# Performance work log

Measured on AMD Instinct MI355X. Metric: run time of the kernel, lower is better.

Reference implementation:

```python
import jax, jax.numpy as jnp
from jax import lax
import numpy as np

D_MODEL = 96; D_STATE = 16; SSM_RATIO = 2.0; D_CONV = 3; K = 4
D_INNER = int(SSM_RATIO * D_MODEL)      # 192
DT_RANK = -(-D_MODEL // 16)             # ceil(96/16) = 6
B_SZ = 4; H = 32; W = 32

# ---- zig-zag (snake) index helpers (static numpy) ----
def _snake_h(Hh, Ww):
    idx = np.tile(np.arange(Ww), (Hh, 1)); idx[1::2] = idx[1::2, ::-1]; return idx  # (H,W)

def _snake_v(Hh, Ww):
    idx = np.tile(np.arange(Hh)[:, None], (1, Ww)); idx[:, 1::2] = idx[::-1, 1::2]; return idx  # (H,W)

def _h_scan(x, d):
    Hh, Ww = x.shape[-2:]
    if d == 'left':
        x = jnp.flip(x, (-1, -2))
    return x[:, :, np.arange(Hh)[:, None], _snake_h(Hh, Ww)]

def _v_scan(x, d):
    Bb, Cc, Hh, Ww = x.shape
    if d == 'up':
        x = jnp.flip(x, (-1, -2))
    t = x[:, :, _snake_v(Hh, Ww), np.arange(Ww)[None, :]]  # gather along H per column
    return jnp.swapaxes(t, -1, -2).reshape(Bb, Cc, Hh, Ww)

def _h_merge(x, d):
    Hh, Ww = x.shape[-2:]
    t = x[:, :, np.arange(Hh)[:, None], _snake_h(Hh, Ww)]
    if d == 'left':
        t = jnp.flip(t, (-1, -2))
    return t

def _v_merge(x, d):
    Hh, Ww = x.shape[-2:]
    t2 = jnp.swapaxes(x, -1, -2)  # (B,C,W,H); requires H==W like the torch source
    t = t2[:, :, _snake_v(Hh, Ww), np.arange(Ww)[None, :]]
    if d == 'up':
        t = jnp.flip(t, (-1, -2))
    return t

def cross_scan(x):
    return jnp.stack([_v_scan(x, 'down'), _v_scan(x, 'up'), _h_scan(x, 'right'), _h_scan(x, 'left')], axis=1)

def cross_merge(ys):
    return (_v_merge(ys[:, 0], 'down') + _v_merge(ys[:, 1], 'up')
            + _h_merge(ys[:, 2], 'right') + _h_merge(ys[:, 3], 'left'))

def selective_scan(u, delta, A, Bs, Cs, Dp, delta_bias):
    # u,delta:(B,K,D,L)  A:(K,D,N)  Bs,Cs:(B,K,N,L)  Dp,delta_bias:(K,D)
    delta = jax.nn.softplus(delta + delta_bias[None, :, :, None])
    dA = jnp.exp(jnp.einsum('bkdl,kdn->lbkdn', delta, A))
    dBu = jnp.einsum('bkdl,bkdl,bknl->lbkdn', delta, u, Bs)
    Ct = jnp.moveaxis(Cs, -1, 0)  # (L,B,K,N)
    def step(h, inp):
        dA_t, dBu_t, c_t = inp
        h = dA_t * h + dBu_t
        return h, jnp.einsum('bkdn,bkn->bkd', h, c_t)
    h0 = jnp.zeros(dA.shape[1:], u.dtype)
    _, ys = lax.scan(step, h0, (dA, dBu, Ct))
    return jnp.moveaxis(ys, 0, -1) + Dp[None, :, :, None] * u  # (B,K,D,L)

def setup_inputs() -> dict:
    key = jax.random.key(0)
    ks = jax.random.split(key, 8)
    x = jax.random.normal(ks[0], (B_SZ, D_MODEL, H, W), jnp.float32)
    in_proj_w = jax.random.normal(ks[1], (2 * D_INNER, D_MODEL), jnp.float32) * (D_MODEL ** -0.5)
    conv_w = jax.random.normal(ks[2], (D_INNER, 1, D_CONV, D_CONV), jnp.float32) * 0.2  # depthwise
    conv_b = jnp.zeros((D_INNER,), jnp.float32)
    x_proj_w = jax.random.normal(ks[3], (K, DT_RANK + 2 * D_STATE, D_INNER), jnp.float32) * (D_INNER ** -0.5)
    s = DT_RANK ** -0.5
    dt_w = jax.random.uniform(ks[4], (K, D_INNER, DT_RANK), jnp.float32, -s, s)
    dt = jax.random.uniform(ks[5], (K, D_INNER), jnp.float32, 0.001, 0.1)
    dt_b = jnp.log(jnp.expm1(dt))  # inverse softplus, as in dt_init
    A_logs = jnp.tile(jnp.log(jnp.arange(1, D_STATE + 1, dtype=jnp.float32)), (K * D_INNER, 1))
    Ds = jnp.ones((K * D_INNER,), jnp.float32)
    gn_gamma = jnp.ones((D_INNER,), jnp.float32)
    gn_beta = jnp.zeros((D_INNER,), jnp.float32)
    out_proj_w = jax.random.normal(ks[6], (D_MODEL, D_INNER), jnp.float32) * (D_INNER ** -0.5)
    return {'x': x, 'in_proj_w': in_proj_w, 'conv_w': conv_w, 'conv_b': conv_b,
            'x_proj_w': x_proj_w, 'dt_w': dt_w, 'dt_b': dt_b, 'A_logs': A_logs, 'Ds': Ds,
            'gn_gamma': gn_gamma, 'gn_beta': gn_beta, 'out_proj_w': out_proj_w}

def reference(x, in_proj_w, conv_w, conv_b, x_proj_w, dt_w, dt_b, A_logs, Ds, gn_gamma, gn_beta, out_proj_w):
    Bb, _, Hh, Ww = x.shape; L = Hh * Ww
    xz = jnp.einsum('bchw,oc->bohw', x, in_proj_w)          # in_proj (1x1 conv, no bias)
    xx, z = jnp.split(xz, 2, axis=1)
    z = jax.nn.silu(z)
    xx = lax.conv_general_dilated(xx, conv_w, (1, 1), 'SAME', feature_group_count=D_INNER,
                                  dimension_numbers=('NCHW', 'OIHW', 'NCHW')) + conv_b[None, :, None, None]
    xx = jax.nn.silu(xx)
    xs = cross_scan(xx).reshape(Bb, K, D_INNER, L)          # 4-direction zig-zag scan
    x_dbl = jnp.einsum('bkdl,kcd->bkcl', xs, x_proj_w)
    dts = jnp.einsum('bkrl,kdr->bkdl', x_dbl[:, :, :DT_RANK], dt_w)
    Bs = x_dbl[:, :, DT_RANK:DT_RANK + D_STATE]
    Cs = x_dbl[:, :, DT_RANK + D_STATE:]
    A = -jnp.exp(A_logs).reshape(K, D_INNER, D_STATE)
    y = selective_scan(xs, dts, A, Bs, Cs, Ds.reshape(K, D_INNER), dt_b)
    y = cross_merge(y.reshape(Bb, K, D_INNER, Hh, Ww))       # (B,D,H,W)
    # out_norm: GroupNorm(1, d_inner) == layernorm over (C,H,W) per sample
    mu = jnp.mean(y, axis=(1, 2, 3), keepdims=True)
    var = jnp.var(y, axis=(1, 2, 3), keepdims=True)
    y = (y - mu) * lax.rsqrt(var + 1e-6)
    y = y * gn_gamma[None, :, None, None] + gn_beta[None, :, None, None]
    y = y * z
    return jnp.einsum('bchw,oc->bohw', y, out_proj_w)
```

## Files before the change

### kernel.cpp

```cpp
#include <hip/hip_runtime.h>
#include <math.h>

#define Bsz 4
#define DM 96
#define DI 192
#define NS 16
#define RK 6
#define KK 4
#define HH 32
#define WW 32
#define LL 1024
#define NC 32
#define CS 32

__device__ __forceinline__ float silu_f(float x) { return x / (1.f + __expf(-x)); }

__device__ __forceinline__ int hw_of_l(int k, int l) {
    int a = l >> 5, r = l & 31;
    int m = (a & 1) ? 31 - r : r;
    int h, w;
    if (k < 2) { w = a; h = m; }
    else       { h = a; w = m; }
    if (k & 1) { h = 31 - h; w = 31 - w; }
    return h * 32 + w;
}

__global__ void in_proj_k(const float* __restrict__ x, const float* __restrict__ w,
                          float* __restrict__ xx, float* __restrict__ zs,
                          float* __restrict__ stats) {
    int bi = blockIdx.x;
    int t = threadIdx.x;
    if (bi == 0 && t < 2 * Bsz) stats[t] = 0.f;
    int lb = bi & 3;
    int og = (bi >> 2) % 96;
    int b = bi / 384;
    int l = lb * 256 + t;
    const float* xb = x + (size_t)b * DM * LL + l;
    float acc[4];
#pragma unroll
    for (int g = 0; g < 4; g++) acc[g] = 0.f;
    for (int c = 0; c < DM; c++) {
        float xv = xb[(size_t)c * LL];
#pragma unroll
        for (int g = 0; g < 4; g++)
            acc[g] = fmaf(xv, w[(size_t)(og * 4 + g) * DM + c], acc[g]);
    }
#pragma unroll
    for (int g = 0; g < 4; g++) {
        int o = og * 4 + g;
        if (o < DI) xx[((size_t)b * DI + o) * LL + l] = acc[g];
        else        zs[((size_t)b * DI + (o - DI)) * LL + l] = silu_f(acc[g]);
    }
}

__global__ void convT_k(const float* __restrict__ xx, const float* __restrict__ cw,
                        const float* __restrict__ cb, float* __restrict__ xxT) {
    __shared__ float tile[32][33];
    int bi = blockIdx.x;
    int h0 = bi % 32;
    int dt = (bi / 32) % 6;
    int b = bi / 192;
    int d0 = dt * 32;
    int t = threadIdx.x;
    int wi = t & 31, dg = t >> 5;

#pragma unroll
    for (int pass = 0; pass < 4; pass++) {
        int di = pass * 8 + dg;
        int d = d0 + di;
        const float* xp = xx + ((size_t)b * DI + d) * LL;
        const float* wp = cw + d * 9;
        float acc = cb[d];
#pragma unroll
        for (int kh = 0; kh < 3; kh++) {
            int hh = h0 + kh - 1;
            if (hh < 0 || hh >= HH) continue;
#pragma unroll
            for (int kw = 0; kw < 3; kw++) {
                int ww2 = wi + kw - 1;
                if (ww2 < 0 || ww2 >= WW) continue;
                acc = fmaf(xp[hh * WW + ww2], wp[kh * 3 + kw], acc);
            }
        }
        tile[wi][di] = silu_f(acc);
    }
    __syncthreads();

    int di = t & 31, w8 = t >> 5;
#pragma unroll
    for (int rep = 0; rep < 4; rep++) {
        int w2 = rep * 8 + w8;
        xxT[((size_t)b * LL + h0 * 32 + w2) * DI + d0 + di] = tile[w2][di];
    }
}

__global__ void __launch_bounds__(512)
xdbl_k(const float* __restrict__ xxT, const float* __restrict__ xpw,
       float* __restrict__ xdbl) {
    __shared__ float tile[64 * 193];
    int blk = blockIdx.x;
    int bk = blk >> 4, lt = blk & 15;
    int k = bk & 3, b = bk >> 2;
    int t = threadIdx.x;

    const float* xb = xxT + (size_t)b * LL * DI;
#pragma unroll
    for (int i = 0; i < 6; i++) {
        int j4 = t + i * 512;
        int lr = j4 / 48;
        int d4 = j4 % 48;
        int hw = hw_of_l(k, lt * 64 + lr);
        float4 v = ((const float4*)(xb + (size_t)hw * DI))[d4];
        float* dst = &tile[lr * 193 + d4 * 4];
        dst[0] = v.x; dst[1] = v.y; dst[2] = v.z; dst[3] = v.w;
    }
    __syncthreads();

    int ll = t & 63;
    int cg = t >> 6;
    int c0 = cg * 5;
    int wlim = (c0 + 5 <= 38) ? 5 : (38 - c0);
    const float* wk = xpw + (size_t)k * 38 * DI;

    float acc[5];
#pragma unroll
    for (int j = 0; j < 5; j++) acc[j] = 0.f;
    const float* xrow = &tile[ll * 193];
#pragma unroll 4
    for (int d = 0; d < DI; d++) {
        float xv = xrow[d];
#pragma unroll
        for (int j = 0; j < 5; j++) {
            int cc = c0 + j; cc = (cc > 37) ? 37 : cc;
            acc[j] = fmaf(xv, wk[(size_t)cc * DI + d], acc[j]);
        }
    }
    float* orow = xdbl + ((size_t)bk * LL + lt * 64 + ll) * 38;
#pragma unroll
    for (int j = 0; j < 5; j++)
        if (j < wlim) orow[c0 + j] = acc[j];
}

#define XDP 40

__global__ void scan_p1(const float* __restrict__ xxT, const float* __restrict__ xdbl,
                        const float* __restrict__ dtw_g, const float* __restrict__ dtb_g,
                        const float* __restrict__ Alog,
                        float* __restrict__ Pst, float* __restrict__ Hloc) {
    __shared__ float u_tile[CS * 192];
    __shared__ float xd_tile[CS * XDP];
    int blk = blockIdx.x;
    int bk = blk / NC, c = blk % NC;
    int k = bk & 3, b = bk >> 2;
    int t = threadIdx.x;

    const float* xb = xxT + (size_t)b * LL * DI;
#pragma unroll
    for (int i = 0; i < 8; i++) {
        int j4 = t + i * 192;
        int s = j4 / 48, d4 = j4 % 48;
        int hw = hw_of_l(k, c * CS + s);
        float4 v = ((const float4*)(xb + (size_t)hw * DI))[d4];
        ((float4*)(&u_tile[s * 192]))[d4] = v;
    }
    const float* xdsrc = xdbl + ((size_t)bk * LL + c * CS) * 38;
    for (int i = t; i < CS * 38; i += 192) {
        int s = i / 38, j = i - s * 38;
        int pj = (j < 6) ? 32 + j : j - 6;
        xd_tile[s * XDP + pj] = xdsrc[i];
    }
    __syncthreads();

    int d = t;
    int kd = k * DI + d;
    float A0 = -__expf(Alog[(size_t)kd * NS]);
    bool pw = true;
#pragma unroll
    for (int n = 1; n < NS; n++) {
        float An = -__expf(Alog[(size_t)kd * NS + n]);
        pw = pw && (fabsf(An - (float)(n + 1) * A0) <= 1e-4f * (float)(n + 1));
    }
    float dtw[RK];
#pragma unroll
    for (int r = 0; r < RK; r++) dtw[r] = dtw_g[(size_t)kd * RK + r];
    float dtb = dtb_g[kd];

    float h[NS], P[NS];
#pragma unroll
    for (int n = 0; n < NS; n++) h[n] = 0.f;

    if (pw) {
        float R = 1.f;
        for (int s = 0; s < CS; s++) {
            const float4* xr = (const float4*)(&xd_tile[s * XDP]);
            float4 b0 = xr[0], b1 = xr[1], b2 = xr[2], b3 = xr[3];
            float4 q0 = xr[8], q1 = xr[9];
            float bb[16];
            bb[0]=b0.x; bb[1]=b0.y; bb[2]=b0.z; bb[3]=b0.w;
            bb[4]=b1.x; bb[5]=b1.y; bb[6]=b1.z; bb[7]=b1.w;
            bb[8]=b2.x; bb[9]=b2.y; bb[10]=b2.z; bb[11]=b2.w;
            bb[12]=b3.x; bb[13]=b3.y; bb[14]=b3.z; bb[15]=b3.w;
            float dt = dtb;
            dt = fmaf(q0.x, dtw[0], dt); dt = fmaf(q0.y, dtw[1], dt);
            dt = fmaf(q0.z, dtw[2], dt); dt = fmaf(q0.w, dtw[3], dt);
            dt = fmaf(q1.x, dtw[4], dt); dt = fmaf(q1.y, dtw[5], dt);
            dt = (dt > 20.f) ? dt : __logf(1.f + __expf(dt));
            float du = dt * u_tile[s * 192 + d];
            float r1 = __expf(dt * A0);
            float r2 = r1 * r1, r4 = r2 * r2, r8 = r4 * r4;
            float aa[16];
            aa[0] = r1; aa[1] = r2; aa[2] = r1 * r2; aa[3] = r4;
#pragma unroll
            for (int n = 0; n < 4; n++) aa[n + 4] = aa[n] * r4;
#pragma unroll
            for (int n = 0; n < 8; n++) aa[n + 8] = aa[n] * r8;
#pragma unroll
            for (int n = 0; n < NS; n++) h[n] = fmaf(aa[n], h[n], du * bb[n]);
            R *= r1;
        }
        float R2 = R * R, R4 = R2 * R2, R8 = R4 * R4;
        P[0] = R; P[1] = R2; P[2] = R * R2; P[3] = R4;
#pragma unroll
        for (int n = 0; n < 4; n++) P[n + 4] = P[n] * R4;
        P[7] = R8;
#pragma unroll
        for (int n = 0; n < 8; n++) P[n + 8] = P[n] * R8;
    } else {
        float A[NS];
#pragma unroll
        for (int n = 0; n < NS; n++) A[n] = -__expf(Alog[(size_t)kd * NS + n]);
#pragma unroll
        for (int n = 0; n < NS; n++) P[n] = 1.f;
        for (int s = 0; s < CS; s++) {
            const float4* xr = (const float4*)(&xd_tile[s * XDP]);
            float4 b0 = xr[0], b1 = xr[1], b2 = xr[2], b3 = xr[3];
            float4 q0 = xr[8], q1 = xr[9];
            float bb[16];
            bb[0]=b0.x; bb[1]=b0.y; bb[2]=b0.z; bb[3]=b0.w;
            bb[4]=b1.x; bb[5]=b1.y; bb[6]=b1.z; bb[7]=b1.w;
            bb[8]=b2.x; bb[9]=b2.y; bb[10]=b2.z; bb[11]=b2.w;
            bb[12]=b3.x; bb[13]=b3.y; bb[14]=b3.z; bb[15]=b3.w;
            float dt = dtb;
            dt = fmaf(q0.x, dtw[0], dt); dt = fmaf(q0.y, dtw[1], dt);
            dt = fmaf(q0.z, dtw[2], dt); dt = fmaf(q0.w, dtw[3], dt);
            dt = fmaf(q1.x, dtw[4], dt); dt = fmaf(q1.y, dtw[5], dt);
            dt = (dt > 20.f) ? dt : __logf(1.f + __expf(dt));
            float du = dt * u_tile[s * 192 + d];
#pragma unroll
            for (int n = 0; n < NS; n++) {
                float a = __expf(dt * A[n]);
                h[n] = fmaf(a, h[n], du * bb[n]);
                P[n] *= a;
            }
        }
    }
    if (c < NC - 1) {
        size_t base = ((size_t)blk * DI + d) * NS;
#pragma unroll
        for (int n = 0; n < NS; n++) { Pst[base + n] = P[n]; Hloc[base + n] = h[n]; }
    }
}

__global__ void scan_mid(const float* __restrict__ Pst, float* __restrict__ Hloc) {
    int gid = blockIdx.x * 256 + threadIdx.x;
    int bk = gid / 1536;
    int j = gid % 1536;
    const float2* Pp = (const float2*)(Pst + (size_t)bk * NC * (DI * NS)) + j;
    float2* Hp = (float2*)(Hloc + (size_t)bk * NC * (DI * NS)) + j;
    const int S = (DI * NS) / 2;

    float2 h = make_float2(0.f, 0.f);
    float2 P[4], L[4];
#pragma unroll
    for (int q = 0; q < 4; q++) { P[q] = Pp[(size_t)q * S]; L[q] = Hp[(size_t)q * S]; }
    for (int c = 0; c < NC; c += 4) {
        float2 Pn[4], Ln[4];
        if (c + 4 < NC) {
#pragma unroll
            for (int q = 0; q < 4; q++) {
                Pn[q] = Pp[(size_t)(c + 4 + q) * S];
                Ln[q] = Hp[(size_t)(c + 4 + q) * S];
            }
        }
#pragma unroll
        for (int q = 0; q < 4; q++) {
            Hp[(size_t)(c + q) * S] = h;
            h.x = fmaf(P[q].x, h.x, L[q].x);
            h.y = fmaf(P[q].y, h.y, L[q].y);
        }
#pragma unroll
        for (int q = 0; q < 4; q++) { P[q] = Pn[q]; L[q] = Ln[q]; }
    }
}

__global__ void scan_p3(const float* __restrict__ xxT, const float* __restrict__ xdbl,
                        const float* __restrict__ dtw_g, const float* __restrict__ dtb_g,
                        const float* __restrict__ Alog, const float* __restrict__ Ds,
                        const float* __restrict__ Hin, float* __restrict__ ysm) {
    __shared__ float u_tile[CS * 192];
    __shared__ float xd_tile[CS * XDP];
    int blk = blockIdx.x;
    int bk = blk / NC, c = blk % NC;
    int k = bk & 3, b = bk >> 2;
    int t = threadIdx.x;

    const float* xb = xxT + (size_t)b * LL * DI;
#pragma unroll
    for (int i = 0; i < 8; i++) {
        int j4 = t + i * 192;
        int s = j4 / 48, d4 = j4 % 48;
        int hw = hw_of_l(k, c * CS + s);
        float4 v = ((const float4*)(xb + (size_t)hw * DI))[d4];
        ((float4*)(&u_tile[s * 192]))[d4] = v;
    }
    const float* xdsrc = xdbl + ((size_t)bk * LL + c * CS) * 38;
    for (int i = t; i < CS * 38; i += 192) {
        int s = i / 38, j = i - s * 38;
        int pj = (j < 6) ? 32 + j : j - 6;
        xd_tile[s * XDP + pj] = xdsrc[i];
    }
    __syncthreads();

    int d = t;
    int kd = k * DI + d;
    float A0 = -__expf(Alog[(size_t)kd * NS]);
    bool pw = true;
#pragma unroll
    for (int n = 1; n < NS; n++) {
        float An = -__expf(Alog[(size_t)kd * NS + n]);
        pw = pw && (fabsf(An - (float)(n + 1) * A0) <= 1e-4f * (float)(n + 1));
    }
    float dtw[RK];
#pragma unroll
    for (int r = 0; r < RK; r++) dtw[r] = dtw_g[(size_t)kd * RK + r];
    float dtb = dtb_g[kd];
    float Dp = Ds[kd];

    float h[NS];
    size_t hbase = ((size_t)blk * DI + d) * NS;
#pragma unroll
    for (int n = 0; n < NS; n++) h[n] = Hin[hbase + n];

    float* yk = ysm + (size_t)bk * LL * DI;

    if (pw) {
        for (int s = 0; s < CS; s++) {
            const float4* xr = (const float4*)(&xd_tile[s * XDP]);
            float4 b0 = xr[0], b1 = xr[1], b2 = xr[2], b3 = xr[3];
            float4 c0 = xr[4], c1 = xr[5], c2 = xr[6], c3 = xr[7];
            float4 q0 = xr[8], q1 = xr[9];
            float bb[16], cf[16];
            bb[0]=b0.x; bb[1]=b0.y; bb[2]=b0.z; bb[3]=b0.w;
            bb[4]=b1.x; bb[5]=b1.y; bb[6]=b1.z; bb[7]=b1.w;
            bb[8]=b2.x; bb[9]=b2.y; bb[10]=b2.z; bb[11]=b2.w;
            bb[12]=b3.x; bb[13]=b3.y; bb[14]=b3.z; bb[15]=b3.w;
            cf[0]=c0.x; cf[1]=c0.y; cf[2]=c0.z; cf[3]=c0.w;
            cf[4]=c1.x; cf[5]=c1.y; cf[6]=c1.z; cf[7]=c1.w;
            cf[8]=c2.x; cf[9]=c2.y; cf[10]=c2.z; cf[11]=c2.w;
            cf[12]=c3.x; cf[13]=c3.y; cf[14]=c3.z; cf[15]=c3.w;
            float dt = dtb;
            dt = fmaf(q0.x, dtw[0], dt); dt = fmaf(q0.y, dtw[1], dt);
            dt = fmaf(q0.z, dtw[2], dt); dt = fmaf(q0.w, dtw[3], dt);
            dt = fmaf(q1.x, dtw[4], dt); dt = fmaf(q1.y, dtw[5], dt);
            dt = (dt > 20.f) ? dt : __logf(1.f + __expf(dt));
            float u = u_tile[s * 192 + d];
            float du = dt * u;
            float r1 = __expf(dt * A0);
            float r2 = r1 * r1, r4 = r2 * r2, r8 = r4 * r4;
            float aa[16];
            aa[0] = r1; aa[1] = r2; aa[2] = r1 * r2; aa[3] = r4;
#pragma unroll
            for (int n = 0; n < 4; n++) aa[n + 4] = aa[n] * r4;
#pragma unroll
            for (int n = 0; n < 8; n++) aa[n + 8] = aa[n] * r8;
            float y = 0.f;
#pragma unroll
            for (int n = 0; n < NS; n++) {
                h[n] = fmaf(aa[n], h[n], du * bb[n]);
                y = fmaf(h[n], cf[n], y);
            }
            int hw = hw_of_l(k, c * CS + s);
            yk[(size_t)hw * DI + d] = fmaf(Dp, u, y);
        }
    } else {
        float A[NS];
#pragma unroll
        for (int n = 0; n < NS; n++) A[n] = -__expf(Alog[(size_t)kd * NS + n]);
        for (int s = 0; s < CS; s++) {
            const float4* xr = (const float4*)(&xd_tile[s * XDP]);
            float4 b0 = xr[0], b1 = xr[1], b2 = xr[2], b3 = xr[3];
            float4 c0 = xr[4], c1 = xr[5], c2 = xr[6], c3 = xr[7];
            float4 q0 = xr[8], q1 = xr[9];
            float bb[16], cf[16];
            bb[0]=b0.x; bb[1]=b0.y; bb[2]=b0.z; bb[3]=b0.w;
            bb[4]=b1.x; bb[5]=b1.y; bb[6]=b1.z; bb[7]=b1.w;
            bb[8]=b2.x; bb[9]=b2.y; bb[10]=b2.z; bb[11]=b2.w;
            bb[12]=b3.x; bb[13]=b3.y; bb[14]=b3.z; bb[15]=b3.w;
            cf[0]=c0.x; cf[1]=c0.y; cf[2]=c0.z; cf[3]=c0.w;
            cf[4]=c1.x; cf[5]=c1.y; cf[6]=c1.z; cf[7]=c1.w;
            cf[8]=c2.x; cf[9]=c2.y; cf[10]=c2.z; cf[11]=c2.w;
            cf[12]=c3.x; cf[13]=c3.y; cf[14]=c3.z; cf[15]=c3.w;
            float dt = dtb;
            dt = fmaf(q0.x, dtw[0], dt); dt = fmaf(q0.y, dtw[1], dt);
            dt = fmaf(q0.z, dtw[2], dt); dt = fmaf(q0.w, dtw[3], dt);
            dt = fmaf(q1.x, dtw[4], dt); dt = fmaf(q1.y, dtw[5], dt);
            dt = (dt > 20.f) ? dt : __logf(1.f + __expf(dt));
            float u = u_tile[s * 192 + d];
            float du = dt * u;
            float y = 0.f;
#pragma unroll
            for (int n = 0; n < NS; n++) {
                float a = __expf(dt * A[n]);
                h[n] = fmaf(a, h[n], du * bb[n]);
                y = fmaf(h[n], cf[n], y);
            }
            int hw = hw_of_l(k, c * CS + s);
            yk[(size_t)hw * DI + d] = fmaf(Dp, u, y);
        }
    }
}

#define MT 8
__global__ void merge_k(const float* __restrict__ ysm, float* __restrict__ ym,
                        float* __restrict__ stats) {
    __shared__ float tile[MT][DI + 1];
    __shared__ float sh1[3], sh2[3];
    int b = blockIdx.y;
    int hw0 = blockIdx.x * MT;
    int d = threadIdx.x;
    const float* yb = ysm + (size_t)b * KK * LL * DI;

    float s1 = 0.f, s2 = 0.f;
#pragma unroll
    for (int hwi = 0; hwi < MT; hwi++) {
        int hw = hw0 + hwi;
        float v = yb[((size_t)0 * LL + hw) * DI + d]
                + yb[((size_t)1 * LL + hw) * DI + d]
                + yb[((size_t)2 * LL + hw) * DI + d]
                + yb[((size_t)3 * LL + hw) * DI + d];
        tile[hwi][d] = v;
        s1 += v; s2 = fmaf(v, v, s2);
    }
#pragma unroll
    for (int off = 32; off > 0; off >>= 1) {
        s1 += __shfl_down(s1, off);
        s2 += __shfl_down(s2, off);
    }
    int lane = threadIdx.x & 63, wid = threadIdx.x >> 6;
    if (lane == 0) { sh1[wid] = s1; sh2[wid] = s2; }
    __syncthreads();
    if (threadIdx.x == 0) {
        atomicAdd(&stats[b * 2],     sh1[0] + sh1[1] + sh1[2]);
        atomicAdd(&stats[b * 2 + 1], sh2[0] + sh2[1] + sh2[2]);
    }
#pragma unroll
    for (int rep = 0; rep < MT; rep++) {
        int j = rep * DI + threadIdx.x;
        int d2 = j >> 3;
        int hwi = j & (MT - 1);
        ym[((size_t)b * DI + d2) * LL + hw0 + hwi] = tile[hwi][d2];
    }
}

__global__ void outz_k(const float* __restrict__ ym, const float* __restrict__ zs,
                       const float* __restrict__ g, const float* __restrict__ be,
                       const float* __restrict__ stats, const float* __restrict__ wo,
                       float* __restrict__ out) {
    int bi = blockIdx.x;
    int t = threadIdx.x;
    int lb = bi & 3;
    int og = (bi >> 2) % 32;
    int b = bi / 128;
    int l = lb * 256 + t;

    const float Ninv = 1.f / (float)(DI * LL);
    float mu = stats[b * 2] * Ninv;
    float var = stats[b * 2 + 1] * Ninv - mu * mu;
    float rstd = rsqrtf(var + 1e-6f);

    const float* yb = ym + (size_t)b * DI * LL + l;
    const float* zb = zs + (size_t)b * DI * LL + l;
    float acc[3];
#pragma unroll
    for (int gg = 0; gg < 3; gg++) acc[gg] = 0.f;
    for (int c = 0; c < DI; c++) {
        float v = (yb[(size_t)c * LL] - mu) * rstd * g[c] + be[c];
        float yv = v * zb[(size_t)c * LL];
#pragma unroll
        for (int gg = 0; gg < 3; gg++)
            acc[gg] = fmaf(yv, wo[(size_t)(og * 3 + gg) * DI + c], acc[gg]);
    }
#pragma unroll
    for (int gg = 0; gg < 3; gg++)
        out[((size_t)b * DM + og * 3 + gg) * LL + l] = acc[gg];
}

extern "C" void kernel_launch(void* const* d_in, const int* in_sizes, int n_in,
                              void* d_out, int out_size, void* d_ws, size_t ws_size,
                              hipStream_t stream) {
    const float* x    = (const float*)d_in[0];
    const float* ipw  = (const float*)d_in[1];
    const float* cw   = (const float*)d_in[2];
    const float* cb   = (const float*)d_in[3];
    const float* xpw  = (const float*)d_in[4];
    const float* dtw  = (const float*)d_in[5];
    const float* dtb  = (const float*)d_in[6];
    const float* Alog = (const float*)d_in[7];
    const float* Ds   = (const float*)d_in[8];
    const float* gng  = (const float*)d_in[9];
    const float* gnb  = (const float*)d_in[10];
    const float* opw  = (const float*)d_in[11];
    float* out = (float*)d_out;

    float* ws = (float*)d_ws;
    const size_t NPH  = (size_t)Bsz * KK * NC * DI * NS;
    const size_t o_xx   = 0;
    const size_t o_zs   = o_xx   + (size_t)Bsz * DI * LL;
    const size_t o_xxT  = o_zs   + (size_t)Bsz * DI * LL;
    const size_t o_xdbl = o_xxT  + (size_t)Bsz * LL * DI;
    const size_t o_P    = o_xdbl + (size_t)Bsz * KK * LL * 38;
    const size_t o_H    = o_P    + NPH;
    const size_t o_ysm  = o_H    + NPH;
    const size_t o_st   = o_ysm  + (size_t)Bsz * KK * LL * DI;

    float* xx    = ws + o_xx;
    float* zs    = ws + o_zs;
    float* xxT   = ws + o_xxT;
    float* xdbl  = ws + o_xdbl;
    float* Pst   = ws + o_P;
    float* Hst   = ws + o_H;
    float* ysm   = ws + o_ysm;
    float* stats = ws + o_st;
    float* ym = xx;

    hipLaunchKernelGGL(in_proj_k, dim3(1536), dim3(256), 0, stream, x, ipw, xx, zs, stats);
    hipLaunchKernelGGL(convT_k, dim3(768), dim3(256), 0, stream, xx, cw, cb, xxT);
    hipLaunchKernelGGL(xdbl_k, dim3(256), dim3(512), 0, stream, xxT, xpw, xdbl);
    hipLaunchKernelGGL(scan_p1, dim3(Bsz * KK * NC), dim3(192), 0, stream,
                       xxT, xdbl, dtw, dtb, Alog, Pst, Hst);
    hipLaunchKernelGGL(scan_mid, dim3(96), dim3(256), 0, stream, Pst, Hst);
    hipLaunchKernelGGL(scan_p3, dim3(Bsz * KK * NC), dim3(192), 0, stream,
                       xxT, xdbl, dtw, dtb, Alog, Ds, Hst, ysm);
    hipLaunchKernelGGL(merge_k, dim3(LL / MT, Bsz), dim3(192), 0, stream, ysm, ym, stats);
    hipLaunchKernelGGL(outz_k, dim3(512), dim3(256), 0, stream, ym, zs, gng, gnb, stats, opw, out);
}
```

Measured before the change: 190.6 us.

## Fuse x_proj computation into both scan passes, drop xdbl kernel

After: 213.1 us. 11.8% more time.

```diff
diff --git a/kernel.cpp b/kernel.cpp
--- a/kernel.cpp
+++ b/kernel.cpp
@@ -94,56 +94,9 @@
     }
 }
 
-__global__ void __launch_bounds__(512)
-xdbl_k(const float* __restrict__ xxT, const float* __restrict__ xpw,
-       float* __restrict__ xdbl) {
-    __shared__ float tile[64 * 193];
-    int blk = blockIdx.x;
-    int bk = blk >> 4, lt = blk & 15;
-    int k = bk & 3, b = bk >> 2;
-    int t = threadIdx.x;
-
-    const float* xb = xxT + (size_t)b * LL * DI;
-#pragma unroll
-    for (int i = 0; i < 6; i++) {
-        int j4 = t + i * 512;
-        int lr = j4 / 48;
-        int d4 = j4 % 48;
-        int hw = hw_of_l(k, lt * 64 + lr);
-        float4 v = ((const float4*)(xb + (size_t)hw * DI))[d4];
-        float* dst = &tile[lr * 193 + d4 * 4];
-        dst[0] = v.x; dst[1] = v.y; dst[2] = v.z; dst[3] = v.w;
-    }
-    __syncthreads();
-
-    int ll = t & 63;
-    int cg = t >> 6;
-    int c0 = cg * 5;
-    int wlim = (c0 + 5 <= 38) ? 5 : (38 - c0);
-    const float* wk = xpw + (size_t)k * 38 * DI;
-
-    float acc[5];
-#pragma unroll
-    for (int j = 0; j < 5; j++) acc[j] = 0.f;
-    const float* xrow = &tile[ll * 193];
-#pragma unroll 4
-    for (int d = 0; d < DI; d++) {
-        float xv = xrow[d];
-#pragma unroll
-        for (int j = 0; j < 5; j++) {
-            int cc = c0 + j; cc = (cc > 37) ? 37 : cc;
-            acc[j] = fmaf(xv, wk[(size_t)cc * DI + d], acc[j]);
-        }
-    }
-    float* orow = xdbl + ((size_t)bk * LL + lt * 64 + ll) * 38;
-#pragma unroll
-    for (int j = 0; j < 5; j++)
-        if (j < wlim) orow[c0 + j] = acc[j];
-}
-
 #define XDP 40
 
-__global__ void scan_p1(const float* __restrict__ xxT, const float* __restrict__ xdbl,
+__global__ void scan_p1(const float* __restrict__ xxT, const float* __restrict__ xpw,
                         const float* __restrict__ dtw_g, const float* __restrict__ dtb_g,
                         const float* __restrict__ Alog,
                         float* __restrict__ Pst, float* __restrict__ Hloc) {
@@ -163,11 +116,37 @@
         float4 v = ((const float4*)(xb + (size_t)hw * DI))[d4];
         ((float4*)(&u_tile[s * 192]))[d4] = v;
     }
-    const float* xdsrc = xdbl + ((size_t)bk * LL + c * CS) * 38;
-    for (int i = t; i < CS * 38; i += 192) {
-        int s = i / 38, j = i - s * 38;
-        int pj = (j < 6) ? 32 + j : j - 6;
-        xd_tile[s * XDP + pj] = xdsrc[i];
+    {
+        int s = t & 31, cg5 = t >> 5;
+        int c0 = cg5 * 7;
+        int wlim = (c0 + 7 <= 38) ? 7 : (38 - c0);
+        const float* wk = xpw + (size_t)k * 38 * DI;
+        int hw = hw_of_l(k, c * CS + s);
+        const float4* urow = (const float4*)(xb + (size_t)hw * DI);
+        float acc[7];
+#pragma unroll
+        for (int j = 0; j < 7; j++) acc[j] = 0.f;
+#pragma unroll 4
+        for (int d4 = 0; d4 < 48; d4++) {
+            float4 uv = urow[d4];
+#pragma unroll
+            for (int j = 0; j < 7; j++) {
+                int cc = c0 + j; cc = (cc > 37) ? 37 : cc;
+                float4 wv = ((const float4*)(wk + (size_t)cc * DI))[d4];
+                acc[j] = fmaf(uv.x, wv.x, acc[j]);
+                acc[j] = fmaf(uv.y, wv.y, acc[j]);
+                acc[j] = fmaf(uv.z, wv.z, acc[j]);
+                acc[j] = fmaf(uv.w, wv.w, acc[j]);
+            }
+        }
+#pragma unroll
+        for (int j = 0; j < 7; j++) {
+            if (j < wlim) {
+                int cc = c0 + j;
+                int pj = (cc < 6) ? 32 + cc : cc - 6;
+                xd_tile[s * XDP + pj] = acc[j];
+            }
+        }
     }
     __syncthreads();
 
@@ -293,7 +272,7 @@
     }
 }
 
-__global__ void scan_p3(const float* __restrict__ xxT, const float* __restrict__ xdbl,
+__global__ void scan_p3(const float* __restrict__ xxT, const float* __restrict__ xpw,
                         const float* __restrict__ dtw_g, const float* __restrict__ dtb_g,
                         const float* __restrict__ Alog, const float* __restrict__ Ds,
                         const float* __restrict__ Hin, float* __restrict__ ysm) {
@@ -313,11 +292,37 @@
         float4 v = ((const float4*)(xb + (size_t)hw * DI))[d4];
         ((float4*)(&u_tile[s * 192]))[d4] = v;
     }
-    const float* xdsrc = xdbl + ((size_t)bk * LL + c * CS) * 38;
-    for (int i = t; i < CS * 38; i += 192) {
-        int s = i / 38, j = i - s * 38;
-        int pj = (j < 6) ? 32 + j : j - 6;
-        xd_tile[s * XDP + pj] = xdsrc[i];
+    {
+        int s = t & 31, cg5 = t >> 5;
+        int c0 = cg5 * 7;
+        int wlim = (c0 + 7 <= 38) ? 7 : (38 - c0);
+        const float* wk = xpw + (size_t)k * 38 * DI;
+        int hw = hw_of_l(k, c * CS + s);
+        const float4* urow = (const float4*)(xb + (size_t)hw * DI);
+        float acc[7];
+#pragma unroll
+        for (int j = 0; j < 7; j++) acc[j] = 0.f;
+#pragma unroll 4
+        for (int d4 = 0; d4 < 48; d4++) {
+            float4 uv = urow[d4];
+#pragma unroll
+            for (int j = 0; j < 7; j++) {
+                int cc = c0 + j; cc = (cc > 37) ? 37 : cc;
+                float4 wv = ((const float4*)(wk + (size_t)cc * DI))[d4];
+                acc[j] = fmaf(uv.x, wv.x, acc[j]);
+                acc[j] = fmaf(uv.y, wv.y, acc[j]);
+                acc[j] = fmaf(uv.z, wv.z, acc[j]);
+                acc[j] = fmaf(uv.w, wv.w, acc[j]);
+            }
+        }
+#pragma unroll
+        for (int j = 0; j < 7; j++) {
+            if (j < wlim) {
+                int cc = c0 + j;
+                int pj = (cc < 6) ? 32 + cc : cc - 6;
+                xd_tile[s * XDP + pj] = acc[j];
+            }
+        }
     }
     __syncthreads();
 
@@ -517,8 +522,7 @@
     const size_t o_xx   = 0;
     const size_t o_zs   = o_xx   + (size_t)Bsz * DI * LL;
     const size_t o_xxT  = o_zs   + (size_t)Bsz * DI * LL;
-    const size_t o_xdbl = o_xxT  + (size_t)Bsz * LL * DI;
-    const size_t o_P    = o_xdbl + (size_t)Bsz * KK * LL * 38;
+    const size_t o_P    = o_xxT  + (size_t)Bsz * LL * DI;
     const size_t o_H    = o_P    + NPH;
     const size_t o_ysm  = o_H    + NPH;
     const size_t o_st   = o_ysm  + (size_t)Bsz * KK * LL * DI;
@@ -526,7 +530,6 @@
     float* xx    = ws + o_xx;
     float* zs    = ws + o_zs;
     float* xxT   = ws + o_xxT;
-    float* xdbl  = ws + o_xdbl;
     float* Pst   = ws + o_P;
     float* Hst   = ws + o_H;
     float* ysm   = ws + o_ysm;
@@ -535,12 +538,11 @@
 
     hipLaunchKernelGGL(in_proj_k, dim3(1536), dim3(256), 0, stream, x, ipw, xx, zs, stats);
     hipLaunchKernelGGL(convT_k, dim3(768), dim3(256), 0, stream, xx, cw, cb, xxT);
-    hipLaunchKernelGGL(xdbl_k, dim3(256), dim3(512), 0, stream, xxT, xpw, xdbl);
     hipLaunchKernelGGL(scan_p1, dim3(Bsz * KK * NC), dim3(192), 0, stream,
-                       xxT, xdbl, dtw, dtb, Alog, Pst, Hst);
+                       xxT, xpw, dtw, dtb, Alog, Pst, Hst);
     hipLaunchKernelGGL(scan_mid, dim3(96), dim3(256), 0, stream, Pst, Hst);
     hipLaunchKernelGGL(scan_p3, dim3(Bsz * KK * NC), dim3(192), 0, stream,
-                       xxT, xdbl, dtw, dtb, Alog, Ds, Hst, ysm);
+                       xxT, xpw, dtw, dtb, Alog, Ds, Hst, ysm);
     hipLaunchKernelGGL(merge_k, dim3(LL / MT, Bsz), dim3(192), 0, stream, ysm, ym, stats);
     hipLaunchKernelGGL(outz_k, dim3(512), dim3(256), 0, stream, ym, zs, gng, gnb, stats, opw, out);
 }
```
